# Optimization experiments

Measured on AMD Instinct MI355X. Metric: run time of the kernel, lower is better.

The kernel has to match this reference:

```python
import jax, jax.numpy as jnp
import numpy as np
import math

B, S, IN_DIM = 4, 2048, 256
ATT_DIM, NUM_HEADS, TOP_K = 128, 4, 32


def _linear_params(key, out_dim, in_dim):
    kw, kb = jax.random.split(key)
    bound = 1.0 / math.sqrt(in_dim)
    w = jax.random.uniform(kw, (out_dim, in_dim), jnp.float32, -bound, bound)
    b = jax.random.uniform(kb, (out_dim,), jnp.float32, -bound, bound)
    return w, b


def setup_inputs() -> dict:
    key = jax.random.key(0)
    keys = jax.random.split(key, 16)
    x = jax.random.normal(keys[0], (B, S, IN_DIM), jnp.float32)
    tp_w, tp_b = _linear_params(keys[1], ATT_DIM, IN_DIM)
    sp_w, sp_b = _linear_params(keys[2], ATT_DIM, IN_DIM)
    ta_qw, ta_qb = _linear_params(keys[3], ATT_DIM, ATT_DIM)
    ta_kw, ta_kb = _linear_params(keys[4], ATT_DIM, ATT_DIM)
    ta_vw, ta_vb = _linear_params(keys[5], ATT_DIM, ATT_DIM)
    ta_ow, ta_ob = _linear_params(keys[6], ATT_DIM, ATT_DIM)
    sa_qw, sa_qb = _linear_params(keys[7], ATT_DIM, ATT_DIM)
    sa_kw, sa_kb = _linear_params(keys[8], ATT_DIM, ATT_DIM)
    sa_vw, sa_vb = _linear_params(keys[9], ATT_DIM, ATT_DIM)
    sa_ow, sa_ob = _linear_params(keys[10], ATT_DIM, ATT_DIM)
    gate_w, gate_b = _linear_params(keys[11], ATT_DIM, 2 * ATT_DIM)
    fus_w, fus_b = _linear_params(keys[12], ATT_DIM, 2 * ATT_DIM)
    return dict(x=x, tp_w=tp_w, tp_b=tp_b, sp_w=sp_w, sp_b=sp_b,
                ta_qw=ta_qw, ta_qb=ta_qb, ta_kw=ta_kw, ta_kb=ta_kb,
                ta_vw=ta_vw, ta_vb=ta_vb, ta_ow=ta_ow, ta_ob=ta_ob,
                sa_qw=sa_qw, sa_qb=sa_qb, sa_kw=sa_kw, sa_kb=sa_kb,
                sa_vw=sa_vw, sa_vb=sa_vb, sa_ow=sa_ow, sa_ob=sa_ob,
                gate_w=gate_w, gate_b=gate_b, fus_w=fus_w, fus_b=fus_b)


def _lin(x, w, b):
    return x @ w.T + b


def _sparse_topk_attention(x, qw, qb, kw, kb, vw, vb, ow, ob):
    # x: [B, S, E]; dropout is identity in eval mode
    b, s, e = x.shape
    h, d = NUM_HEADS, e // NUM_HEADS
    q = _lin(x, qw, qb).reshape(b, s, h, d).transpose(0, 2, 1, 3)  # [B,H,S,D]
    k = _lin(x, kw, kb).reshape(b, s, h, d).transpose(0, 2, 1, 3)
    v = _lin(x, vw, vb).reshape(b, s, h, d).transpose(0, 2, 1, 3)
    scores = jnp.einsum('bhqd,bhkd->bhqk', q, k) / math.sqrt(d)  # [B,H,S,S]
    kk = min(TOP_K, s)
    top_scores, top_idx = jax.lax.top_k(scores, kk)  # [B,H,S,K]
    soft = jax.nn.softmax(top_scores, axis=-1)
    # scatter softmaxed top-k weights into a zero [B,H,S,S] matrix (faithful to source)
    bi = jnp.arange(b)[:, None, None, None]
    hi = jnp.arange(h)[None, :, None, None]
    si = jnp.arange(s)[None, None, :, None]
    sparse = jnp.zeros_like(scores).at[bi, hi, si, top_idx].set(soft)
    out = jnp.einsum('bhqk,bhkd->bhqd', sparse, v)
    out = out.transpose(0, 2, 1, 3).reshape(b, s, e)
    return _lin(out, ow, ob)


def reference(x, tp_w, tp_b, sp_w, sp_b,
              ta_qw, ta_qb, ta_kw, ta_kb, ta_vw, ta_vb, ta_ow, ta_ob,
              sa_qw, sa_qb, sa_kw, sa_kb, sa_vw, sa_vb, sa_ow, sa_ob,
              gate_w, gate_b, fus_w, fus_b):
    temporal = _lin(x, tp_w, tp_b)
    temporal = _sparse_topk_attention(temporal, ta_qw, ta_qb, ta_kw, ta_kb,
                                      ta_vw, ta_vb, ta_ow, ta_ob)
    semantic = _lin(x, sp_w, sp_b)
    semantic = _sparse_topk_attention(semantic, sa_qw, sa_qb, sa_kw, sa_kb,
                                      sa_vw, sa_vb, sa_ow, sa_ob)
    concat = jnp.concatenate([temporal, semantic], axis=-1)  # [B,S,2A]
    gate = jax.nn.sigmoid(_lin(concat, gate_w, gate_b))
    fused = _lin(concat, fus_w, fus_b) * gate
    return fused
```

## Files before the change

kernel.cpp:

```cpp
#include <hip/hip_runtime.h>
#include <math.h>

#define B_   4
#define S_   2048
#define AD   128
#define NH   4
#define HD   32
#define TK   32
#define SEG  1048576
#define CAP  192

#define OFF_PROJ 0
#define OFF_Q    (1 * SEG)
#define OFF_K    (2 * SEG)
#define OFF_V    (3 * SEG)
#define OFF_ATT  (4 * SEG)
#define OFF_T    (5 * SEG)
#define OFF_SB   (6 * SEG)
#define OFF_CAT  (7 * SEG)

__device__ float g_ws[9 * SEG];
__device__ float g_sc[16 * S_ * S_];

__device__ __forceinline__ unsigned f2key(float s) {
    unsigned u = __float_as_uint(s);
    return (u & 0x80000000u) ? ~u : (u | 0x80000000u);
}
__device__ __forceinline__ float key2f(unsigned k) {
    unsigned u = (k & 0x80000000u) ? (k & 0x7FFFFFFFu) : ~k;
    return __uint_as_float(u);
}

template <int KD>
__global__ __launch_bounds__(256)
void lin_kernel(const float* __restrict__ Xext, int xoff,
                const float* __restrict__ W, const float* __restrict__ Bv,
                int yoff)
{
    const float* X = Xext ? Xext : (const float*)(g_ws + xoff);
    float* Y = g_ws + yoff;
    __shared__ float Xs[64][33];
    __shared__ float Ws[64][33];
    const int bm = blockIdx.x * 64;
    const int bn = blockIdx.y * 64;
    const int t  = threadIdx.x;
    const int tx = t & 15, ty = t >> 4;
    float acc[4][4] = {};
    for (int kk = 0; kk < KD; kk += 32) {
        #pragma unroll
        for (int i = 0; i < 8; ++i) {
            int idx = t + i * 256;
            int r = idx >> 5, c = idx & 31;
            Xs[r][c] = X[(size_t)(bm + r) * KD + kk + c];
            Ws[r][c] = W[(size_t)(bn + r) * KD + kk + c];
        }
        __syncthreads();
        #pragma unroll
        for (int kc = 0; kc < 32; ++kc) {
            float a[4], bb[4];
            #pragma unroll
            for (int i = 0; i < 4; ++i) a[i] = Xs[ty * 4 + i][kc];
            #pragma unroll
            for (int j = 0; j < 4; ++j) bb[j] = Ws[tx * 4 + j][kc];
            #pragma unroll
            for (int i = 0; i < 4; ++i)
                #pragma unroll
                for (int j = 0; j < 4; ++j)
                    acc[i][j] = fmaf(a[i], bb[j], acc[i][j]);
        }
        __syncthreads();
    }
    #pragma unroll
    for (int i = 0; i < 4; ++i) {
        int row = bm + ty * 4 + i;
        #pragma unroll
        for (int j = 0; j < 4; ++j) {
            int col = bn + tx * 4 + j;
            Y[(size_t)row * AD + col] = acc[i][j] + Bv[col];
        }
    }
}

template <int KD>
__global__ __launch_bounds__(256)
void lin3_kernel(int xoff,
                 const float* __restrict__ W0, const float* __restrict__ B0, int y0,
                 const float* __restrict__ W1, const float* __restrict__ B1, int y1,
                 const float* __restrict__ W2, const float* __restrict__ B2, int y2)
{
    const int z = blockIdx.z;
    const float* X = (const float*)(g_ws + xoff);
    const float* W = (z == 0) ? W0 : (z == 1) ? W1 : W2;
    const float* Bv = (z == 0) ? B0 : (z == 1) ? B1 : B2;
    float* Y = g_ws + ((z == 0) ? y0 : (z == 1) ? y1 : y2);
    __shared__ float Xs[64][33];
    __shared__ float Ws[64][33];
    const int bm = blockIdx.x * 64;
    const int bn = blockIdx.y * 64;
    const int t  = threadIdx.x;
    const int tx = t & 15, ty = t >> 4;
    float acc[4][4] = {};
    for (int kk = 0; kk < KD; kk += 32) {
        #pragma unroll
        for (int i = 0; i < 8; ++i) {
            int idx = t + i * 256;
            int r = idx >> 5, c = idx & 31;
            Xs[r][c] = X[(size_t)(bm + r) * KD + kk + c];
            Ws[r][c] = W[(size_t)(bn + r) * KD + kk + c];
        }
        __syncthreads();
        #pragma unroll
        for (int kc = 0; kc < 32; ++kc) {
            float a[4], bb[4];
            #pragma unroll
            for (int i = 0; i < 4; ++i) a[i] = Xs[ty * 4 + i][kc];
            #pragma unroll
            for (int j = 0; j < 4; ++j) bb[j] = Ws[tx * 4 + j][kc];
            #pragma unroll
            for (int i = 0; i < 4; ++i)
                #pragma unroll
                for (int j = 0; j < 4; ++j)
                    acc[i][j] = fmaf(a[i], bb[j], acc[i][j]);
        }
        __syncthreads();
    }
    #pragma unroll
    for (int i = 0; i < 4; ++i) {
        int row = bm + ty * 4 + i;
        #pragma unroll
        for (int j = 0; j < 4; ++j) {
            int col = bn + tx * 4 + j;
            Y[(size_t)row * AD + col] = acc[i][j] + Bv[col];
        }
    }
}

__global__ __launch_bounds__(256)
void score_kernel(int qoff, int koff)
{
    const int bh = blockIdx.z, b = bh >> 2, h = bh & 3;
    const float* Q = g_ws + qoff + (size_t)b * S_ * AD + h * HD;
    const float* K = g_ws + koff + (size_t)b * S_ * AD + h * HD;
    float* Sc = g_sc + (size_t)bh * S_ * S_;
    __shared__ float Qs[64][33];
    __shared__ float Ks[64][33];
    const int t = threadIdx.x, tx = t & 15, ty = t >> 4;
    const int q0 = blockIdx.y * 64, k0 = blockIdx.x * 64;
    #pragma unroll
    for (int i = 0; i < 8; ++i) {
        int idx = t + i * 256;
        int r = idx >> 5, c = idx & 31;
        Qs[r][c] = Q[(size_t)(q0 + r) * AD + c];
        Ks[r][c] = K[(size_t)(k0 + r) * AD + c];
    }
    __syncthreads();
    float acc[4][4] = {};
    #pragma unroll
    for (int kc = 0; kc < 32; ++kc) {
        float a[4], bb[4];
        #pragma unroll
        for (int i = 0; i < 4; ++i) a[i] = Qs[ty * 4 + i][kc];
        #pragma unroll
        for (int j = 0; j < 4; ++j) bb[j] = Ks[tx * 4 + j][kc];
        #pragma unroll
        for (int i = 0; i < 4; ++i)
            #pragma unroll
            for (int j = 0; j < 4; ++j)
                acc[i][j] = fmaf(a[i], bb[j], acc[i][j]);
    }
    const float scale = 0.17677669529663688f;
    #pragma unroll
    for (int i = 0; i < 4; ++i) {
        float4 o;
        o.x = acc[i][0] * scale; o.y = acc[i][1] * scale;
        o.z = acc[i][2] * scale; o.w = acc[i][3] * scale;
        *(float4*)(Sc + (size_t)(q0 + ty * 4 + i) * S_ + k0 + tx * 4) = o;
    }
}

__global__ __launch_bounds__(256)
void topk_kernel(int voff, int ooff)
{
    const float* V = g_ws + voff;
    float* O = g_ws + ooff;

    __shared__ unsigned long long sve[4][CAP];
    __shared__ float    wsel[4][32];
    __shared__ unsigned jsel[4][32];

    const int wid  = threadIdx.x >> 6;
    const int lane = threadIdx.x & 63;
    const int gr   = blockIdx.x * 4 + wid;
    const int bh   = gr >> 11, q = gr & 2047;
    const int b    = bh >> 2,  h = bh & 3;

    unsigned long long* sv = sve[wid];
    float*    wp = wsel[wid];
    unsigned* jp = jsel[wid];

    const float* Srow  = g_sc + (size_t)bh * S_ * S_ + (size_t)q * S_;
    const float* vbase = V + (size_t)b * S_ * AD + h * HD;

    unsigned keys[32];
    unsigned lmax = 0u;
    #pragma unroll
    for (int i = 0; i < 8; ++i) {
        float4 s4 = ((const float4*)Srow)[i * 64 + lane];
        unsigned k0 = f2key(s4.x), k1 = f2key(s4.y);
        unsigned k2 = f2key(s4.z), k3 = f2key(s4.w);
        keys[i * 4 + 0] = k0; keys[i * 4 + 1] = k1;
        keys[i * 4 + 2] = k2; keys[i * 4 + 3] = k3;
        unsigned m01 = (k0 > k1) ? k0 : k1;
        unsigned m23 = (k2 > k3) ? k2 : k3;
        unsigned m = (m01 > m23) ? m01 : m23;
        lmax = (m > lmax) ? m : lmax;
    }

    unsigned bs = lmax;
    #pragma unroll
    for (int k = 2; k <= 64; k <<= 1) {
        #pragma unroll
        for (int j = k >> 1; j > 0; j >>= 1) {
            unsigned o = (unsigned)__shfl_xor((int)bs, j);
            bool up = ((lane & k) == 0);
            bool lower = ((lane & j) == 0);
            bs = (up == lower) ? (bs < o ? bs : o) : (bs > o ? bs : o);
        }
    }
    const unsigned thr  = (unsigned)__shfl((int)bs, 32);
    const unsigned mkey = (unsigned)__shfl((int)bs, 63);
    const float Mf = key2f(mkey);

    int base = 0;
    const unsigned long long lt = (1ull << lane) - 1ull;
    #pragma unroll
    for (int t = 0; t < 32; ++t) {
        bool pred = keys[t] >= thr;
        unsigned long long m = __ballot(pred);
        int slot = base + __popcll(m & lt);
        if (pred && slot < CAP) {
            unsigned jidx = (unsigned)((t >> 2) * 256 + lane * 4 + (t & 3));
            sv[slot] = ((unsigned long long)keys[t] << 32) | (unsigned)(2047 - jidx);
        }
        base += __popcll(m);
    }
    const int S = base;
    asm volatile("s_waitcnt lgkmcnt(0)" ::: "memory");

    if (S <= 64) {
        unsigned long long pi = (lane < S) ? sv[lane] : 0ull;
        int rank = 0;
        for (int jx = 0; jx < S; ++jx)
            rank += (sv[jx] > pi) ? 1 : 0;
        float e = 0.f; unsigned ji = 0;
        if (lane < S && rank < TK) {
            float val = key2f((unsigned)(pi >> 32));
            e = __expf(val - Mf);
            ji = 2047u - (unsigned)(pi & 0xFFFFFFFFull);
        }
        float esum = e;
        #pragma unroll
        for (int off = 1; off < 64; off <<= 1) esum += __shfl_xor(esum, off);
        if (lane < S && rank < TK) { wp[rank] = e / esum; jp[rank] = ji; }
    } else if (S <= CAP) {
        unsigned long long pi[3]; int rk[3]; float ee[3]; unsigned jj[3];
        float esum = 0.f;
        #pragma unroll
        for (int u = 0; u < 3; ++u) {
            int i = lane + u * 64;
            pi[u] = (i < S) ? sv[i] : 0ull;
            rk[u] = 0; ee[u] = 0.f; jj[u] = 0;
        }
        for (int jx = 0; jx < S; ++jx) {
            unsigned long long pj = sv[jx];
            #pragma unroll
            for (int u = 0; u < 3; ++u)
                rk[u] += (pj > pi[u]) ? 1 : 0;
        }
        #pragma unroll
        for (int u = 0; u < 3; ++u) {
            int i = lane + u * 64;
            if (i < S && rk[u] < TK) {
                float val = key2f((unsigned)(pi[u] >> 32));
                ee[u] = __expf(val - Mf);
                jj[u] = 2047u - (unsigned)(pi[u] & 0xFFFFFFFFull);
                esum += ee[u];
            }
        }
        #pragma unroll
        for (int off = 1; off < 64; off <<= 1) esum += __shfl_xor(esum, off);
        #pragma unroll
        for (int u = 0; u < 3; ++u) {
            int i = lane + u * 64;
            if (i < S && rk[u] < TK) { wp[rk[u]] = ee[u] / esum; jp[rk[u]] = jj[u]; }
        }
    } else {
        unsigned consumed = 0u;
        for (int i = 0; i < TK; ++i) {
            unsigned bk = 0u; unsigned gj = 0xFFFFFFFFu;
            #pragma unroll
            for (int t = 0; t < 32; ++t) {
                if (((consumed >> t) & 1u) == 0u) {
                    unsigned kk = keys[t];
                    unsigned j = (unsigned)((t >> 2) * 256 + lane * 4 + (t & 3));
                    if (kk > bk || (kk == bk && j < gj)) { bk = kk; gj = j; }
                }
            }
            #pragma unroll
            for (int off = 1; off < 64; off <<= 1) {
                unsigned ok = (unsigned)__shfl_xor((int)bk, off);
                unsigned oj = (unsigned)__shfl_xor((int)gj, off);
                if (ok > bk || (ok == bk && oj < gj)) { bk = ok; gj = oj; }
            }
            if (((gj >> 2) & 63u) == (unsigned)lane && gj != 0xFFFFFFFFu) {
                int t = ((int)gj >> 8) * 4 + ((int)gj & 3);
                consumed |= (1u << t);
            }
            if (lane == 0) { wp[i] = key2f(bk); jp[i] = gj; }
        }
        asm volatile("s_waitcnt lgkmcnt(0)" ::: "memory");
        float v = (lane < TK) ? wp[lane] : 0.f;
        float e = (lane < TK) ? __expf(v - Mf) : 0.f;
        float esum = e;
        #pragma unroll
        for (int off = 1; off < 64; off <<= 1) esum += __shfl_xor(esum, off);
        if (lane < TK) wp[lane] = e / esum;
    }
    asm volatile("s_waitcnt lgkmcnt(0)" ::: "memory");

    float oacc = 0.f;
    const int dd = lane & 31, half = lane >> 5;
    #pragma unroll
    for (int u2 = 0; u2 < 16; ++u2) {
        int i = half * 16 + u2;
        oacc = fmaf(wp[i], vbase[(size_t)jp[i] * AD + dd], oacc);
    }
    oacc += __shfl_down(oacc, 32);
    if (lane < HD) O[((size_t)b * S_ + q) * AD + h * HD + lane] = oacc;
}

__global__ __launch_bounds__(256)
void concat_kernel()
{
    int i = blockIdx.x * 256 + threadIdx.x;
    int row = i >> 8, c = i & 255;
    float v = (c < AD) ? g_ws[OFF_T + row * AD + c]
                       : g_ws[OFF_SB + row * AD + (c - AD)];
    g_ws[OFF_CAT + i] = v;
}

__global__ __launch_bounds__(256)
void fuse_kernel(float* __restrict__ out)
{
    int i = blockIdx.x * 256 + threadIdx.x;
    float g = g_ws[OFF_Q + i];
    float f = g_ws[OFF_K + i];
    out[i] = f / (1.0f + expf(-g));
}

extern "C" void kernel_launch(void* const* d_in, const int* in_sizes, int n_in,
                              void* d_out, int out_size, void* d_ws, size_t ws_size,
                              hipStream_t stream)
{
    (void)in_sizes; (void)n_in; (void)d_ws; (void)ws_size; (void)out_size;
    const float* x      = (const float*)d_in[0];
    const float* tp_w   = (const float*)d_in[1];
    const float* tp_b   = (const float*)d_in[2];
    const float* sp_w   = (const float*)d_in[3];
    const float* sp_b   = (const float*)d_in[4];
    const float* gate_w = (const float*)d_in[21];
    const float* gate_b = (const float*)d_in[22];
    const float* fus_w  = (const float*)d_in[23];
    const float* fus_b  = (const float*)d_in[24];

    dim3 gl(128, 2);
    for (int br = 0; br < 2; ++br) {
        const float* pw = br ? sp_w : tp_w;
        const float* pb = br ? sp_b : tp_b;
        int base = 5 + br * 8;
        const float* qw = (const float*)d_in[base + 0];
        const float* qb = (const float*)d_in[base + 1];
        const float* kw = (const float*)d_in[base + 2];
        const float* kb = (const float*)d_in[base + 3];
        const float* vw = (const float*)d_in[base + 4];
        const float* vb = (const float*)d_in[base + 5];
        const float* ow = (const float*)d_in[base + 6];
        const float* ob = (const float*)d_in[base + 7];

        lin_kernel<256><<<gl, 256, 0, stream>>>(x, 0, pw, pb, OFF_PROJ);
        lin3_kernel<128><<<dim3(128, 2, 3), 256, 0, stream>>>(
            OFF_PROJ, qw, qb, OFF_Q, kw, kb, OFF_K, vw, vb, OFF_V);
        score_kernel<<<dim3(32, 32, 16), 256, 0, stream>>>(OFF_Q, OFF_K);
        topk_kernel<<<8192, 256, 0, stream>>>(OFF_V, OFF_ATT);
        lin_kernel<128><<<gl, 256, 0, stream>>>(nullptr, OFF_ATT, ow, ob,
                                                br ? OFF_SB : OFF_T);
    }
    concat_kernel<<<8192, 256, 0, stream>>>();
    lin3_kernel<256><<<dim3(128, 2, 2), 256, 0, stream>>>(
        OFF_CAT, gate_w, gate_b, OFF_Q, fus_w, fus_b, OFF_K,
        (const float*)nullptr, (const float*)nullptr, 0);
    fuse_kernel<<<4096, 256, 0, stream>>>((float*)d_out);
}
```

Before: 451.8 us.

## Chunk score buffer by heads and vectorize shared-memory GEMM tiles

Splits score computation and top-k selection into two chunks of 8 batch-heads, halving the score scratch buffer so each chunk's writes may stay cache-resident before the top-k kernel reads them. All GEMM-style kernels now store tiles transposed in shared memory, which allows float4 global loads, float4 shared reads and float4 output stores. The top-k kernel issues all score-row loads before converting them to keys. This costs extra kernel launches and slightly smaller grids per launch.

```diff
diff --git a/kernel.cpp b/kernel.cpp
--- a/kernel.cpp
+++ b/kernel.cpp
@@ -20,7 +20,7 @@
 #define OFF_CAT  (7 * SEG)
 
 __device__ float g_ws[9 * SEG];
-__device__ float g_sc[16 * S_ * S_];
+__device__ float g_sc[8 * S_ * S_];
 
 __device__ __forceinline__ unsigned f2key(float s) {
     unsigned u = __float_as_uint(s);
@@ -39,29 +39,32 @@
 {
     const float* X = Xext ? Xext : (const float*)(g_ws + xoff);
     float* Y = g_ws + yoff;
-    __shared__ float Xs[64][33];
-    __shared__ float Ws[64][33];
+    __shared__ float Xs[32][68];
+    __shared__ float Ws[32][68];
     const int bm = blockIdx.x * 64;
     const int bn = blockIdx.y * 64;
     const int t  = threadIdx.x;
     const int tx = t & 15, ty = t >> 4;
+    const int sr = t >> 3, sc4 = t & 7;
     float acc[4][4] = {};
     for (int kk = 0; kk < KD; kk += 32) {
         #pragma unroll
-        for (int i = 0; i < 8; ++i) {
-            int idx = t + i * 256;
-            int r = idx >> 5, c = idx & 31;
-            Xs[r][c] = X[(size_t)(bm + r) * KD + kk + c];
-            Ws[r][c] = W[(size_t)(bn + r) * KD + kk + c];
+        for (int it = 0; it < 2; ++it) {
+            int rr = sr + it * 32;
+            float4 xa = *(const float4*)(X + (size_t)(bm + rr) * KD + kk + sc4 * 4);
+            float4 wa = *(const float4*)(W + (size_t)(bn + rr) * KD + kk + sc4 * 4);
+            Xs[sc4*4+0][rr] = xa.x; Xs[sc4*4+1][rr] = xa.y;
+            Xs[sc4*4+2][rr] = xa.z; Xs[sc4*4+3][rr] = xa.w;
+            Ws[sc4*4+0][rr] = wa.x; Ws[sc4*4+1][rr] = wa.y;
+            Ws[sc4*4+2][rr] = wa.z; Ws[sc4*4+3][rr] = wa.w;
         }
         __syncthreads();
         #pragma unroll
         for (int kc = 0; kc < 32; ++kc) {
-            float a[4], bb[4];
-            #pragma unroll
-            for (int i = 0; i < 4; ++i) a[i] = Xs[ty * 4 + i][kc];
-            #pragma unroll
-            for (int j = 0; j < 4; ++j) bb[j] = Ws[tx * 4 + j][kc];
+            float4 a4 = *(const float4*)&Xs[kc][ty * 4];
+            float4 b4 = *(const float4*)&Ws[kc][tx * 4];
+            float a[4] = {a4.x, a4.y, a4.z, a4.w};
+            float bb[4] = {b4.x, b4.y, b4.z, b4.w};
             #pragma unroll
             for (int i = 0; i < 4; ++i)
                 #pragma unroll
@@ -73,11 +76,11 @@
     #pragma unroll
     for (int i = 0; i < 4; ++i) {
         int row = bm + ty * 4 + i;
-        #pragma unroll
-        for (int j = 0; j < 4; ++j) {
-            int col = bn + tx * 4 + j;
-            Y[(size_t)row * AD + col] = acc[i][j] + Bv[col];
-        }
+        int col = bn + tx * 4;
+        float4 o;
+        o.x = acc[i][0] + Bv[col + 0]; o.y = acc[i][1] + Bv[col + 1];
+        o.z = acc[i][2] + Bv[col + 2]; o.w = acc[i][3] + Bv[col + 3];
+        *(float4*)(Y + (size_t)row * AD + col) = o;
     }
 }
 
@@ -93,29 +96,32 @@
     const float* W = (z == 0) ? W0 : (z == 1) ? W1 : W2;
     const float* Bv = (z == 0) ? B0 : (z == 1) ? B1 : B2;
     float* Y = g_ws + ((z == 0) ? y0 : (z == 1) ? y1 : y2);
-    __shared__ float Xs[64][33];
-    __shared__ float Ws[64][33];
+    __shared__ float Xs[32][68];
+    __shared__ float Ws[32][68];
     const int bm = blockIdx.x * 64;
     const int bn = blockIdx.y * 64;
     const int t  = threadIdx.x;
     const int tx = t & 15, ty = t >> 4;
+    const int sr = t >> 3, sc4 = t & 7;
     float acc[4][4] = {};
     for (int kk = 0; kk < KD; kk += 32) {
         #pragma unroll
-        for (int i = 0; i < 8; ++i) {
-            int idx = t + i * 256;
-            int r = idx >> 5, c = idx & 31;
-            Xs[r][c] = X[(size_t)(bm + r) * KD + kk + c];
-            Ws[r][c] = W[(size_t)(bn + r) * KD + kk + c];
+        for (int it = 0; it < 2; ++it) {
+            int rr = sr + it * 32;
+            float4 xa = *(const float4*)(X + (size_t)(bm + rr) * KD + kk + sc4 * 4);
+            float4 wa = *(const float4*)(W + (size_t)(bn + rr) * KD + kk + sc4 * 4);
+            Xs[sc4*4+0][rr] = xa.x; Xs[sc4*4+1][rr] = xa.y;
+            Xs[sc4*4+2][rr] = xa.z; Xs[sc4*4+3][rr] = xa.w;
+            Ws[sc4*4+0][rr] = wa.x; Ws[sc4*4+1][rr] = wa.y;
+            Ws[sc4*4+2][rr] = wa.z; Ws[sc4*4+3][rr] = wa.w;
         }
         __syncthreads();
         #pragma unroll
         for (int kc = 0; kc < 32; ++kc) {
-            float a[4], bb[4];
-            #pragma unroll
-            for (int i = 0; i < 4; ++i) a[i] = Xs[ty * 4 + i][kc];
-            #pragma unroll
-            for (int j = 0; j < 4; ++j) bb[j] = Ws[tx * 4 + j][kc];
+            float4 a4 = *(const float4*)&Xs[kc][ty * 4];
+            float4 b4 = *(const float4*)&Ws[kc][tx * 4];
+            float a[4] = {a4.x, a4.y, a4.z, a4.w};
+            float bb[4] = {b4.x, b4.y, b4.z, b4.w};
             #pragma unroll
             for (int i = 0; i < 4; ++i)
                 #pragma unroll
@@ -127,41 +133,45 @@
     #pragma unroll
     for (int i = 0; i < 4; ++i) {
         int row = bm + ty * 4 + i;
-        #pragma unroll
-        for (int j = 0; j < 4; ++j) {
-            int col = bn + tx * 4 + j;
-            Y[(size_t)row * AD + col] = acc[i][j] + Bv[col];
-        }
-    }
-}
-
-__global__ __launch_bounds__(256)
-void score_kernel(int qoff, int koff)
-{
-    const int bh = blockIdx.z, b = bh >> 2, h = bh & 3;
-    const float* Q = g_ws + qoff + (size_t)b * S_ * AD + h * HD;
-    const float* K = g_ws + koff + (size_t)b * S_ * AD + h * HD;
-    float* Sc = g_sc + (size_t)bh * S_ * S_;
-    __shared__ float Qs[64][33];
-    __shared__ float Ks[64][33];
+        int col = bn + tx * 4;
+        float4 o;
+        o.x = acc[i][0] + Bv[col + 0]; o.y = acc[i][1] + Bv[col + 1];
+        o.z = acc[i][2] + Bv[col + 2]; o.w = acc[i][3] + Bv[col + 3];
+        *(float4*)(Y + (size_t)row * AD + col) = o;
+    }
+}
+
+__global__ __launch_bounds__(256)
+void score_kernel(int qoff, int koff, int chunk)
+{
+    const int zh = blockIdx.z;
+    const int hh = chunk * 8 + zh, b = hh >> 2, h = hh & 3;
+    const float* Qb = g_ws + qoff + (size_t)b * S_ * AD + h * HD;
+    const float* Kb = g_ws + koff + (size_t)b * S_ * AD + h * HD;
+    float* Sc = g_sc + (size_t)zh * S_ * S_;
+    __shared__ float Qs[32][68];
+    __shared__ float Ks[32][68];
     const int t = threadIdx.x, tx = t & 15, ty = t >> 4;
+    const int sr = t >> 3, sc4 = t & 7;
     const int q0 = blockIdx.y * 64, k0 = blockIdx.x * 64;
     #pragma unroll
-    for (int i = 0; i < 8; ++i) {
-        int idx = t + i * 256;
-        int r = idx >> 5, c = idx & 31;
-        Qs[r][c] = Q[(size_t)(q0 + r) * AD + c];
-        Ks[r][c] = K[(size_t)(k0 + r) * AD + c];
+    for (int it = 0; it < 2; ++it) {
+        int rr = sr + it * 32;
+        float4 qa = *(const float4*)(Qb + (size_t)(q0 + rr) * AD + sc4 * 4);
+        float4 ka = *(const float4*)(Kb + (size_t)(k0 + rr) * AD + sc4 * 4);
+        Qs[sc4*4+0][rr] = qa.x; Qs[sc4*4+1][rr] = qa.y;
+        Qs[sc4*4+2][rr] = qa.z; Qs[sc4*4+3][rr] = qa.w;
+        Ks[sc4*4+0][rr] = ka.x; Ks[sc4*4+1][rr] = ka.y;
+        Ks[sc4*4+2][rr] = ka.z; Ks[sc4*4+3][rr] = ka.w;
     }
     __syncthreads();
     float acc[4][4] = {};
     #pragma unroll
     for (int kc = 0; kc < 32; ++kc) {
-        float a[4], bb[4];
-        #pragma unroll
-        for (int i = 0; i < 4; ++i) a[i] = Qs[ty * 4 + i][kc];
-        #pragma unroll
-        for (int j = 0; j < 4; ++j) bb[j] = Ks[tx * 4 + j][kc];
+        float4 a4 = *(const float4*)&Qs[kc][ty * 4];
+        float4 b4 = *(const float4*)&Ks[kc][tx * 4];
+        float a[4] = {a4.x, a4.y, a4.z, a4.w};
+        float bb[4] = {b4.x, b4.y, b4.z, b4.w};
         #pragma unroll
         for (int i = 0; i < 4; ++i)
             #pragma unroll
@@ -179,7 +189,7 @@
 }
 
 __global__ __launch_bounds__(256)
-void topk_kernel(int voff, int ooff)
+void topk_kernel(int voff, int ooff, int chunk)
 {
     const float* V = g_ws + voff;
     float* O = g_ws + ooff;
@@ -191,23 +201,26 @@
     const int wid  = threadIdx.x >> 6;
     const int lane = threadIdx.x & 63;
     const int gr   = blockIdx.x * 4 + wid;
-    const int bh   = gr >> 11, q = gr & 2047;
-    const int b    = bh >> 2,  h = bh & 3;
+    const int zh   = gr >> 11, q = gr & 2047;
+    const int hh   = chunk * 8 + zh;
+    const int b    = hh >> 2,  h = hh & 3;
 
     unsigned long long* sv = sve[wid];
     float*    wp = wsel[wid];
     unsigned* jp = jsel[wid];
 
-    const float* Srow  = g_sc + (size_t)bh * S_ * S_ + (size_t)q * S_;
+    const float* Srow  = g_sc + (size_t)zh * S_ * S_ + (size_t)q * S_;
     const float* vbase = V + (size_t)b * S_ * AD + h * HD;
 
+    float4 s4[8];
+    #pragma unroll
+    for (int i = 0; i < 8; ++i) s4[i] = ((const float4*)Srow)[i * 64 + lane];
     unsigned keys[32];
     unsigned lmax = 0u;
     #pragma unroll
     for (int i = 0; i < 8; ++i) {
-        float4 s4 = ((const float4*)Srow)[i * 64 + lane];
-        unsigned k0 = f2key(s4.x), k1 = f2key(s4.y);
-        unsigned k2 = f2key(s4.z), k3 = f2key(s4.w);
+        unsigned k0 = f2key(s4[i].x), k1 = f2key(s4[i].y);
+        unsigned k2 = f2key(s4[i].z), k3 = f2key(s4[i].w);
         keys[i * 4 + 0] = k0; keys[i * 4 + 1] = k1;
         keys[i * 4 + 2] = k2; keys[i * 4 + 3] = k3;
         unsigned m01 = (k0 > k1) ? k0 : k1;
@@ -390,8 +403,10 @@
         lin_kernel<256><<<gl, 256, 0, stream>>>(x, 0, pw, pb, OFF_PROJ);
         lin3_kernel<128><<<dim3(128, 2, 3), 256, 0, stream>>>(
             OFF_PROJ, qw, qb, OFF_Q, kw, kb, OFF_K, vw, vb, OFF_V);
-        score_kernel<<<dim3(32, 32, 16), 256, 0, stream>>>(OFF_Q, OFF_K);
-        topk_kernel<<<8192, 256, 0, stream>>>(OFF_V, OFF_ATT);
+        for (int chunk = 0; chunk < 2; ++chunk) {
+            score_kernel<<<dim3(32, 32, 8), 256, 0, stream>>>(OFF_Q, OFF_K, chunk);
+            topk_kernel<<<4096, 256, 0, stream>>>(OFF_V, OFF_ATT, chunk);
+        }
         lin_kernel<128><<<gl, 256, 0, stream>>>(nullptr, OFF_ATT, ow, ob,
                                                 br ? OFF_SB : OFF_T);
     }
```

Result: faster. 373.3 us (-17.4%).
